# Optimization experiments

Hardware: AMD Instinct MI355X
Metric: run time of the kernel (lower is better)

## Reference

```python
import jax, jax.numpy as jnp
import numpy as np
from jax import lax

B, L, D = 2, 1024, 1024
INTER = 2816  # _find_multiple(round(4.0*1024*2/3), 256)
K, PAD = 3, 1
S = 32  # sqrt(L)
K2 = K * K


def setup_inputs() -> dict:
    key = jax.random.key(0)
    ks = jax.random.split(key, 7)
    x = jax.random.normal(ks[0], (B, L, D), dtype=jnp.float32)
    w_gate_up = jax.random.normal(ks[1], (2 * INTER, D), dtype=jnp.float32) / np.sqrt(D)
    w_metric = jax.random.normal(ks[2], (7, INTER, 3, 3), dtype=jnp.float32) / np.sqrt(INTER * 9)
    b_metric = jax.random.normal(ks[3], (7,), dtype=jnp.float32) * 0.01
    conv_w = jax.random.normal(ks[4], (INTER, 1, K, K), dtype=jnp.float32) / K
    conv_b = jnp.zeros((INTER,), dtype=jnp.float32)
    w_down = jax.random.normal(ks[5], (D, INTER), dtype=jnp.float32) / np.sqrt(INTER)
    return {"x": x, "w_gate_up": w_gate_up, "w_metric": w_metric,
            "b_metric": b_metric, "conv_w": conv_w, "conv_b": conv_b,
            "w_down": w_down}


def _metric_offsets(x2d, w_metric, b_metric):
    # Finsler-Randers style metric: 2x2 linear map M, drift vector, tanh scale.
    p = lax.conv_general_dilated(x2d, w_metric, (1, 1), 'SAME',
                                 dimension_numbers=('NCHW', 'OIHW', 'NCHW'))
    p = p + b_metric[None, :, None, None]  # [B,7,S,S]
    m00, m01, m10, m11 = p[:, 0], p[:, 1], p[:, 2], p[:, 3]
    dr_y, dr_x = p[:, 4], p[:, 5]
    scale = jnp.tanh(p[:, 6])
    ky = (jnp.arange(K) - PAD).astype(x2d.dtype)
    py = jnp.repeat(ky, K)   # (K2,) kernel-tap dy
    px = jnp.tile(ky, K)     # (K2,) kernel-tap dx
    pyb = py[None, :, None, None]
    pxb = px[None, :, None, None]
    off_y = scale[:, None] * (m00[:, None] * pyb + m01[:, None] * pxb) + dr_y[:, None]
    off_x = scale[:, None] * (m10[:, None] * pyb + m11[:, None] * pxb) + dr_x[:, None]
    return off_y, off_x, py, px  # offsets: [B,K2,S,S]


def _deform_depthwise(x2d, off_y, off_x, py, px, conv_w, conv_b):
    # Sampling positions per output pixel & kernel tap: [B,K2,S,S]
    iy = jnp.arange(S, dtype=x2d.dtype)
    pos_y = iy[None, None, :, None] + py[None, :, None, None] + off_y
    pos_x = iy[None, None, None, :] + px[None, :, None, None] + off_x
    y0 = jnp.floor(pos_y)
    x0 = jnp.floor(pos_x)
    ty = pos_y - y0
    tx = pos_x - x0
    y0i = y0.astype(jnp.int32)
    x0i = x0.astype(jnp.int32)
    flat = x2d.reshape(B, INTER, S * S)

    def corner(yy, xx):
        valid = ((yy >= 0) & (yy < S) & (xx >= 0) & (xx < S)).astype(x2d.dtype)
        idx = (jnp.clip(yy, 0, S - 1) * S + jnp.clip(xx, 0, S - 1)).reshape(B, 1, -1)
        v = jnp.take_along_axis(flat, idx, axis=2).reshape(B, INTER, K2, S, S)
        return v * valid[:, None]

    w00 = ((1 - ty) * (1 - tx))[:, None]
    w01 = ((1 - ty) * tx)[:, None]
    w10 = (ty * (1 - tx))[:, None]
    w11 = (ty * tx)[:, None]
    acc = w00 * corner(y0i, x0i)
    acc = acc + w01 * corner(y0i, x0i + 1)
    acc = acc + w10 * corner(y0i + 1, x0i)
    acc = acc + w11 * corner(y0i + 1, x0i + 1)
    out = jnp.einsum('bckij,ck->bcij', acc, conv_w.reshape(INTER, K2))
    return out + conv_b[None, :, None, None]


def reference(x, w_gate_up, w_metric, b_metric, conv_w, conv_b, w_down):
    gu = jnp.einsum('bld,fd->blf', x, w_gate_up)          # [B,L,2*inter]
    gate, up = jnp.split(gu, 2, axis=-1)
    x_ffn = jax.nn.silu(gate) * up                         # [B,L,inter]
    x2d = x_ffn.transpose(0, 2, 1).reshape(B, INTER, S, S)
    off_y, off_x, py, px = _metric_offsets(x2d, w_metric, b_metric)
    out2d = _deform_depthwise(x2d, off_y, off_x, py, px, conv_w, conv_b)
    grid_out = out2d.reshape(B, INTER, L).transpose(0, 2, 1)
    return jnp.einsum('blf,df->bld', grid_out, w_down)
```

## Files before the change

### kernel.cpp

```cpp
#include <hip/hip_runtime.h>
#include <hip/hip_bf16.h>
#include <cstdint>
#include <cstddef>
#include <type_traits>

#define INTER 2816

typedef __bf16 bf16x8 __attribute__((ext_vector_type(8)));
typedef float f32x4 __attribute__((ext_vector_type(4)));
typedef unsigned short u16x8 __attribute__((ext_vector_type(8)));
using bf16 = __hip_bfloat16;
using u16 = unsigned short;

__device__ __forceinline__ u16 f2bu(float f) {
  bf16 h = __float2bfloat16(f);
  return *reinterpret_cast<u16*>(&h);
}
__device__ __forceinline__ float bu2f(u16 u) {
  bf16 h = *reinterpret_cast<bf16*>(&u);
  return __bfloat162float(h);
}

__device__ __forceinline__ void async16(const u16* g, u16* l) {
  __builtin_amdgcn_global_load_lds(
      (const __attribute__((address_space(1))) unsigned int*)g,
      (__attribute__((address_space(3))) unsigned int*)l, 16, 0, 0);
}

__device__ __forceinline__ void stage8(u16* dst, const float* src) {
  const float4 a = *(const float4*)(src);
  const float4 b = *(const float4*)(src + 4);
  u16 tmp[8] = {f2bu(a.x), f2bu(a.y), f2bu(a.z), f2bu(a.w),
                f2bu(b.x), f2bu(b.y), f2bu(b.z), f2bu(b.w)};
  *(uint4*)dst = *(uint4*)tmp;
}

__global__ __launch_bounds__(256)
void prep_all(const float* __restrict__ x, const float* __restrict__ wgu,
              const float* __restrict__ wd, const float* __restrict__ w_metric,
              const float* __restrict__ conv_w, u16* __restrict__ xbf,
              u16* __restrict__ wgubf, u16* __restrict__ wdbf,
              u16* __restrict__ wm2, u16* __restrict__ cwb) {
  constexpr size_t S0 = (size_t)2048 * 1024;
  constexpr size_t S1 = (size_t)5632 * 1024;
  constexpr size_t S2 = (size_t)1024 * 2816;
  constexpr size_t NCONV_THREADS = (S0 + S1 + S2) / 8;
  const size_t t = (size_t)blockIdx.x * 256 + threadIdx.x;
  if (t < NCONV_THREADS) {
    const size_t e0 = t * 8;
    const float* src;
    u16* dst;
    size_t off;
    if (e0 < S0) {
      src = x; dst = xbf; off = e0;
    } else if (e0 < S0 + S1) {
      src = wgu; dst = wgubf; off = e0 - S0;
    } else {
      src = wd; dst = wdbf; off = e0 - S0 - S1;
    }
    stage8(dst + off, src + off);
  } else {
    const unsigned p = (unsigned)(t - NCONV_THREADS);
    const unsigned y = p / 2816u;
    const unsigned c = p - y * 2816u;
    if (y < 64) {
      float v = 0.f;
      if (y < 63) {
        const unsigned o = y / 9, tap = y - o * 9;
        v = w_metric[((size_t)o * INTER + c) * 9 + tap];
      }
      wm2[(size_t)y * INTER + c] = f2bu(v);
    } else {
      const unsigned k = y - 64;
      cwb[(size_t)k * INTER + c] = f2bu(conv_w[(size_t)c * 9 + k]);
    }
  }
}

template <int BN, bool NSWAP, typename OT>
__global__ __launch_bounds__(256, 3)
void gemm_nt(const u16* __restrict__ A, int lda, const u16* __restrict__ Bt,
             int ldb, OT* __restrict__ C, int M, int ldc, int K) {
  constexpr int NJ = BN / 32;
  __shared__ u16 As[2][128 * 32];
  __shared__ u16 Bs[2][BN * 32];
  const size_t koff = (size_t)blockIdx.z * K;
  A += koff;
  Bt += koff;
  C += (size_t)blockIdx.z * M * ldc;
  const int m0 = (NSWAP ? blockIdx.y : blockIdx.x) * 128;
  const int n0 = (NSWAP ? blockIdx.x : blockIdx.y) * BN;
  const int tid = threadIdx.x;
  const int lane = tid & 63;
  const int wv = tid >> 6;
  const int wm = wv & 1, wn = wv >> 1;
  const int lr = lane & 15;
  const int lq = lane >> 4;

  f32x4 acc[4][NJ];
#pragma unroll
  for (int i = 0; i < 4; ++i)
#pragma unroll
    for (int j = 0; j < NJ; ++j) acc[i][j] = (f32x4){0.f, 0.f, 0.f, 0.f};

  const int srow = tid >> 2;
  const int scol = (tid & 3) * 8;
  const u16* gA0 = A + (size_t)(m0 + srow) * lda + scol;
  const u16* gA1 = A + (size_t)(m0 + 64 + srow) * lda + scol;
  const u16* gB0 = Bt + (size_t)(n0 + srow) * ldb + scol;
  const u16* gB1 = Bt + (size_t)(n0 + 64 + srow) * ldb + scol;

  const int nIter = K >> 5;
  async16(gA0, &As[0][tid * 8]);
  async16(gA1, &As[0][2048 + tid * 8]);
  async16(gB0, &Bs[0][tid * 8]);
  if constexpr (BN == 128) async16(gB1, &Bs[0][2048 + tid * 8]);

  for (int it = 0; it < nIter; ++it) {
    __syncthreads();
    const int cur = it & 1;
    const u16* as = As[cur];
    const u16* bs = Bs[cur];
    if (it + 1 < nIter) {
      const int kb = (it + 1) << 5;
      const int nxt = cur ^ 1;
      async16(gA0 + kb, &As[nxt][tid * 8]);
      async16(gA1 + kb, &As[nxt][2048 + tid * 8]);
      async16(gB0 + kb, &Bs[nxt][tid * 8]);
      if constexpr (BN == 128) async16(gB1 + kb, &Bs[nxt][2048 + tid * 8]);
    }
    bf16x8 af[4], bfr[NJ];
#pragma unroll
    for (int i = 0; i < 4; ++i)
      af[i] = *(const bf16x8*)(&as[(wm * 64 + i * 16 + lr) * 32 + lq * 8]);
#pragma unroll
    for (int j = 0; j < NJ; ++j)
      bfr[j] = *(const bf16x8*)(&bs[(wn * (BN / 2) + j * 16 + lr) * 32 + lq * 8]);
#pragma unroll
    for (int i = 0; i < 4; ++i)
#pragma unroll
      for (int j = 0; j < NJ; ++j)
        acc[i][j] = __builtin_amdgcn_mfma_f32_16x16x32_bf16(af[i], bfr[j],
                                                            acc[i][j], 0, 0, 0);
  }

#pragma unroll
  for (int i = 0; i < 4; ++i)
#pragma unroll
    for (int j = 0; j < NJ; ++j) {
      const int col = n0 + wn * (BN / 2) + j * 16 + lr;
#pragma unroll
      for (int r = 0; r < 4; ++r) {
        const int row = m0 + wm * 64 + i * 16 + lq * 4 + r;
        const float v = acc[i][j][r];
        if constexpr (std::is_same_v<OT, float>) {
          C[(size_t)row * ldc + col] = v;
        } else {
          C[(size_t)row * ldc + col] = f2bu(v);
        }
      }
    }
}

__global__ void reduce4(const float* __restrict__ q2, float* __restrict__ out) {
  const size_t i = ((size_t)blockIdx.x * 256 + threadIdx.x) * 4;
  const size_t S = (size_t)2048 * 1024;
  float4 a = *(const float4*)(q2 + i);
  const float4 b = *(const float4*)(q2 + S + i);
  const float4 c = *(const float4*)(q2 + 2 * S + i);
  const float4 d = *(const float4*)(q2 + 3 * S + i);
  a.x += b.x + c.x + d.x;
  a.y += b.y + c.y + d.y;
  a.z += b.z + c.z + d.z;
  a.w += b.w + c.w + d.w;
  *(float4*)(out + i) = a;
}

__global__ __launch_bounds__(256, 2)
void gateup_gemm(const u16* __restrict__ x, const u16* __restrict__ wgu,
                 u16* __restrict__ xffn) {
  constexpr int K = 1024;
  __shared__ u16 As[2][128 * 32];
  __shared__ u16 Bgs[2][64 * 32];
  __shared__ u16 Bus[2][64 * 32];
  const int n0 = blockIdx.x * 64;
  const int m0 = blockIdx.y * 128;
  const int tid = threadIdx.x;
  const int lane = tid & 63;
  const int wv = tid >> 6;
  const int wm = wv & 1, wn = wv >> 1;
  const int lr = lane & 15;
  const int lq = lane >> 4;

  f32x4 accg[4][2], accu[4][2];
#pragma unroll
  for (int i = 0; i < 4; ++i)
#pragma unroll
    for (int j = 0; j < 2; ++j) {
      accg[i][j] = (f32x4){0.f, 0.f, 0.f, 0.f};
      accu[i][j] = (f32x4){0.f, 0.f, 0.f, 0.f};
    }

  const int srow = tid >> 2;
  const int scol = (tid & 3) * 8;
  const u16* gA0 = x + (size_t)(m0 + srow) * K + scol;
  const u16* gA1 = x + (size_t)(m0 + 64 + srow) * K + scol;
  const u16* gBg = wgu + (size_t)(n0 + srow) * K + scol;
  const u16* gBu = wgu + (size_t)(INTER + n0 + srow) * K + scol;

  constexpr int nIter = K >> 5;
  async16(gA0, &As[0][tid * 8]);
  async16(gA1, &As[0][2048 + tid * 8]);
  async16(gBg, &Bgs[0][tid * 8]);
  async16(gBu, &Bus[0][tid * 8]);

  for (int it = 0; it < nIter; ++it) {
    __syncthreads();
    const int cur = it & 1;
    const u16* as = As[cur];
    const u16* bgs = Bgs[cur];
    const u16* bus = Bus[cur];
    if (it + 1 < nIter) {
      const int kb = (it + 1) << 5;
      const int nxt = cur ^ 1;
      async16(gA0 + kb, &As[nxt][tid * 8]);
      async16(gA1 + kb, &As[nxt][2048 + tid * 8]);
      async16(gBg + kb, &Bgs[nxt][tid * 8]);
      async16(gBu + kb, &Bus[nxt][tid * 8]);
    }
    bf16x8 af[4], bg[2], bu[2];
#pragma unroll
    for (int i = 0; i < 4; ++i)
      af[i] = *(const bf16x8*)(&as[(wm * 64 + i * 16 + lr) * 32 + lq * 8]);
#pragma unroll
    for (int j = 0; j < 2; ++j) {
      bg[j] = *(const bf16x8*)(&bgs[(wn * 32 + j * 16 + lr) * 32 + lq * 8]);
      bu[j] = *(const bf16x8*)(&bus[(wn * 32 + j * 16 + lr) * 32 + lq * 8]);
    }
#pragma unroll
    for (int i = 0; i < 4; ++i)
#pragma unroll
      for (int j = 0; j < 2; ++j) {
        accg[i][j] = __builtin_amdgcn_mfma_f32_16x16x32_bf16(af[i], bg[j],
                                                             accg[i][j], 0, 0, 0);
        accu[i][j] = __builtin_amdgcn_mfma_f32_16x16x32_bf16(af[i], bu[j],
                                                             accu[i][j], 0, 0, 0);
      }
  }

#pragma unroll
  for (int i = 0; i < 4; ++i)
#pragma unroll
    for (int j = 0; j < 2; ++j) {
      const int col = n0 + wn * 32 + j * 16 + lr;
#pragma unroll
      for (int r = 0; r < 4; ++r) {
        const int row = m0 + wm * 64 + i * 16 + lq * 4 + r;
        const float g = accg[i][j][r];
        const float u = accu[i][j][r];
        const float s = g / (1.f + __expf(-g));
        xffn[(size_t)row * INTER + col] = f2bu(s * u);
      }
    }
}

__global__ __launch_bounds__(64)
void offsets_fused(const float* __restrict__ q,
                   const float* __restrict__ b_metric,
                   float4* __restrict__ wrec, int4* __restrict__ orec) {
  __shared__ float lds[130 * 65];
  const int chunk = blockIdx.x;
  const int b = chunk >> 4;
  const int c0 = (chunk & 15) * 64;
  const int t = threadIdx.x;

  for (int v = t; v < 130 * 16; v += 64) {
    const int row = v >> 4;
    const int c4 = (v & 15) * 4;
    int pg = c0 - 33 + row;
    pg = min(max(pg, 0), 1023);
    const float* src = q + ((size_t)b * 1024 + pg) * 64 + c4;
    float4 s = *(const float4*)(src);
#pragma unroll
    for (int ks = 1; ks < 8; ++ks) {
      const float4 vv = *(const float4*)(src + (size_t)ks * 2048 * 64);
      s.x += vv.x; s.y += vv.y; s.z += vv.z; s.w += vv.w;
    }
    float* d = &lds[row * 65 + c4];
    d[0] = s.x; d[1] = s.y; d[2] = s.z; d[3] = s.w;
  }
  __syncthreads();

  const int pix = c0 + t;
  const int i = pix >> 5, j = pix & 31;
  float p[7];
#pragma unroll
  for (int o = 0; o < 7; ++o) p[o] = b_metric[o];
#pragma unroll
  for (int tap = 0; tap < 9; ++tap) {
    const int dy = tap / 3 - 1, dx = tap % 3 - 1;
    const int ii = i + dy, jj = j + dx;
    if ((unsigned)ii < 32u && (unsigned)jj < 32u) {
      const float* r = &lds[(t + 33 + dy * 32 + dx) * 65 + tap];
#pragma unroll
      for (int o = 0; o < 7; ++o) p[o] += r[o * 9];
    }
  }
  const float m00 = p[0], m01 = p[1], m10 = p[2], m11 = p[3];
  const float dry = p[4], drx = p[5];
  const float sc = tanhf(p[6]);
#pragma unroll
  for (int k = 0; k < 9; ++k) {
    const float pyk = (float)(k / 3 - 1), pxk = (float)(k % 3 - 1);
    const float offy = sc * (m00 * pyk + m01 * pxk) + dry;
    const float offx = sc * (m10 * pyk + m11 * pxk) + drx;
    const float posy = (float)i + pyk + offy;
    const float posx = (float)j + pxk + offx;
    const float y0f = floorf(posy), x0f = floorf(posx);
    const int y0 = (int)y0f, x0 = (int)x0f;
    const float ty = posy - y0f, tx = posx - x0f;
    const int y1 = y0 + 1, x1 = x0 + 1;
    const float vy0 = ((unsigned)y0 < 32u) ? 1.f : 0.f;
    const float vy1 = ((unsigned)y1 < 32u) ? 1.f : 0.f;
    const float vx0 = ((unsigned)x0 < 32u) ? 1.f : 0.f;
    const float vx1 = ((unsigned)x1 < 32u) ? 1.f : 0.f;
    float4 w;
    w.x = (1.f - ty) * (1.f - tx) * vy0 * vx0;
    w.y = (1.f - ty) * tx * vy0 * vx1;
    w.z = ty * (1.f - tx) * vy1 * vx0;
    w.w = ty * tx * vy1 * vx1;
    const int cy0 = min(max(y0, 0), 31), cy1 = min(max(y1, 0), 31);
    const int cx0 = min(max(x0, 0), 31), cx1 = min(max(x1, 0), 31);
    int4 o;
    o.x = (cy0 * 32 + cx0) * (INTER * 2);
    o.y = (cy0 * 32 + cx1) * (INTER * 2);
    o.z = (cy1 * 32 + cx0) * (INTER * 2);
    o.w = (cy1 * 32 + cx1) * (INTER * 2);
    const size_t r = (((size_t)b * 9 + k) << 10) + pix;
    wrec[r] = w;
    orec[r] = o;
  }
}

__global__ __launch_bounds__(256)
void deform_kernel(const u16* __restrict__ xffn,
                   const float4* __restrict__ wrec,
                   const int4* __restrict__ orec,
                   const u16* __restrict__ cwb,
                   const float* __restrict__ conv_b,
                   u16* __restrict__ gridout) {
  const unsigned t = blockIdx.x * 256 + threadIdx.x;
  const unsigned pix = t / 352u;
  const unsigned cv = t - pix * 352u;
  const int c0 = cv * 8;
  const int b = pix >> 10, l = pix & 1023;

  float acc[8];
  {
    const float4 b0 = *(const float4*)(&conv_b[c0]);
    const float4 b1 = *(const float4*)(&conv_b[c0 + 4]);
    acc[0] = b0.x; acc[1] = b0.y; acc[2] = b0.z; acc[3] = b0.w;
    acc[4] = b1.x; acc[5] = b1.y; acc[6] = b1.z; acc[7] = b1.w;
  }
  const char* xb = (const char*)xffn +
                   ((size_t)b * 1024 * INTER + c0) * sizeof(u16);
#pragma unroll
  for (int k = 0; k < 9; ++k) {
    const size_t r = (((size_t)b * 9 + k) << 10) + l;
    const float4 w = wrec[r];
    const int4 o = orec[r];
    const u16x8 v00 = *(const u16x8*)(xb + o.x);
    const u16x8 v01 = *(const u16x8*)(xb + o.y);
    const u16x8 v10 = *(const u16x8*)(xb + o.z);
    const u16x8 v11 = *(const u16x8*)(xb + o.w);
    const u16x8 cw = *(const u16x8*)(&cwb[(size_t)k * INTER + c0]);
#pragma unroll
    for (int e = 0; e < 8; ++e) {
      const float bl = w.x * bu2f(v00[e]) + w.y * bu2f(v01[e]) +
                       w.z * bu2f(v10[e]) + w.w * bu2f(v11[e]);
      acc[e] += bl * bu2f(cw[e]);
    }
  }
  u16 outv[8];
#pragma unroll
  for (int e = 0; e < 8; ++e) outv[e] = f2bu(acc[e]);
  *(uint4*)(gridout + ((size_t)b * 1024 + l) * INTER + c0) = *(uint4*)outv;
}

extern "C" void kernel_launch(void* const* d_in, const int* in_sizes, int n_in,
                              void* d_out, int out_size, void* d_ws,
                              size_t ws_size, hipStream_t stream) {
  const float* x         = (const float*)d_in[0];
  const float* w_gate_up = (const float*)d_in[1];
  const float* w_metric  = (const float*)d_in[2];
  const float* b_metric  = (const float*)d_in[3];
  const float* conv_w    = (const float*)d_in[4];
  const float* conv_b    = (const float*)d_in[5];
  const float* w_down    = (const float*)d_in[6];
  float* out = (float*)d_out;

  char* w = (char*)d_ws;
  u16* gridout  = (u16*)(w);
  float* q2     = (float*)(w + (12u << 20));
  u16* xffn     = (u16*)(w + (12u << 20));
  u16* xbf      = (u16*)(w + (24u << 20));
  u16* wgubf    = (u16*)(w + (28u << 20) + (256u << 10));
  float* q_conv = (float*)(w + (28u << 20) + (256u << 10));
  u16* wm2      = (u16*)(w + (40u << 20));
  u16* cwb      = (u16*)(w + (41u << 20));
  float4* wrec  = (float4*)(w + (42u << 20));
  int4* orec    = (int4*)(w + (43u << 20));
  u16* wdbf     = (u16*)(w + (44u << 20));

  prep_all<<<6051, 256, 0, stream>>>(x, w_gate_up, w_down, w_metric, conv_w,
                                     xbf, wgubf, wdbf, wm2, cwb);
  gateup_gemm<<<dim3(44, 16), 256, 0, stream>>>(xbf, wgubf, xffn);
  gemm_nt<64, false, float><<<dim3(16, 1, 8), 256, 0, stream>>>(
      xffn, INTER, wm2, INTER, q_conv, 2048, 64, 352);
  offsets_fused<<<32, 64, 0, stream>>>(q_conv, b_metric, wrec, orec);
  deform_kernel<<<2816, 256, 0, stream>>>(xffn, wrec, orec, cwb, conv_b,
                                          gridout);
  gemm_nt<128, true, float><<<dim3(8, 16, 4), 256, 0, stream>>>(
      gridout, INTER, wdbf, INTER, q2, 2048, 1024, 704);
  reduce4<<<2048, 256, 0, stream>>>(q2, out);
}
```

Before: 204.9 us.

## Restructure GEMM k-loops to 64-wide stages, retune split-K, remap deform blocks

Both GEMM kernels replace the double-buffered 32-wide prefetch pipeline with a loop that loads a 64-wide k slab, synchronizes, computes both halves, then synchronizes again. This halves the barrier count per k element but drops the overlap of global loads with MFMA work. The metric-conv GEMM moves from 8 to 11 split-K slices of 256 and the reduction in offsets_fused sums 11 partials to match. The deform kernel permutes its block index so that consecutively launched blocks are spread across pixel ranges, changing scheduling and cache locality.

```diff
diff --git a/kernel.cpp b/kernel.cpp
--- a/kernel.cpp
+++ b/kernel.cpp
@@ -82,8 +82,9 @@
 void gemm_nt(const u16* __restrict__ A, int lda, const u16* __restrict__ Bt,
              int ldb, OT* __restrict__ C, int M, int ldc, int K) {
   constexpr int NJ = BN / 32;
-  __shared__ u16 As[2][128 * 32];
-  __shared__ u16 Bs[2][BN * 32];
+  constexpr int BHALF = BN * 32;
+  __shared__ u16 As[2 * 128 * 32];
+  __shared__ u16 Bs[2 * BHALF];
   const size_t koff = (size_t)blockIdx.z * K;
   A += koff;
   Bt += koff;
@@ -110,38 +111,33 @@
   const u16* gB0 = Bt + (size_t)(n0 + srow) * ldb + scol;
   const u16* gB1 = Bt + (size_t)(n0 + 64 + srow) * ldb + scol;
 
-  const int nIter = K >> 5;
-  async16(gA0, &As[0][tid * 8]);
-  async16(gA1, &As[0][2048 + tid * 8]);
-  async16(gB0, &Bs[0][tid * 8]);
-  if constexpr (BN == 128) async16(gB1, &Bs[0][2048 + tid * 8]);
-
-  for (int it = 0; it < nIter; ++it) {
+  for (int kb = 0; kb < K; kb += 64) {
+#pragma unroll
+    for (int h = 0; h < 2; ++h) {
+      const int kh = kb + h * 32;
+      async16(gA0 + kh, As + h * 4096 + tid * 8);
+      async16(gA1 + kh, As + h * 4096 + 2048 + tid * 8);
+      async16(gB0 + kh, Bs + h * BHALF + tid * 8);
+      if constexpr (BN == 128) async16(gB1 + kh, Bs + h * BHALF + 2048 + tid * 8);
+    }
     __syncthreads();
-    const int cur = it & 1;
-    const u16* as = As[cur];
-    const u16* bs = Bs[cur];
-    if (it + 1 < nIter) {
-      const int kb = (it + 1) << 5;
-      const int nxt = cur ^ 1;
-      async16(gA0 + kb, &As[nxt][tid * 8]);
-      async16(gA1 + kb, &As[nxt][2048 + tid * 8]);
-      async16(gB0 + kb, &Bs[nxt][tid * 8]);
-      if constexpr (BN == 128) async16(gB1 + kb, &Bs[nxt][2048 + tid * 8]);
-    }
-    bf16x8 af[4], bfr[NJ];
-#pragma unroll
-    for (int i = 0; i < 4; ++i)
-      af[i] = *(const bf16x8*)(&as[(wm * 64 + i * 16 + lr) * 32 + lq * 8]);
-#pragma unroll
-    for (int j = 0; j < NJ; ++j)
-      bfr[j] = *(const bf16x8*)(&bs[(wn * (BN / 2) + j * 16 + lr) * 32 + lq * 8]);
-#pragma unroll
-    for (int i = 0; i < 4; ++i)
+#pragma unroll
+    for (int h = 0; h < 2; ++h) {
+      bf16x8 af[4], bfr[NJ];
+#pragma unroll
+      for (int i = 0; i < 4; ++i)
+        af[i] = *(const bf16x8*)(&As[h * 4096 + (wm * 64 + i * 16 + lr) * 32 + lq * 8]);
 #pragma unroll
       for (int j = 0; j < NJ; ++j)
-        acc[i][j] = __builtin_amdgcn_mfma_f32_16x16x32_bf16(af[i], bfr[j],
-                                                            acc[i][j], 0, 0, 0);
+        bfr[j] = *(const bf16x8*)(&Bs[h * BHALF + (wn * (BN / 2) + j * 16 + lr) * 32 + lq * 8]);
+#pragma unroll
+      for (int i = 0; i < 4; ++i)
+#pragma unroll
+        for (int j = 0; j < NJ; ++j)
+          acc[i][j] = __builtin_amdgcn_mfma_f32_16x16x32_bf16(af[i], bfr[j],
+                                                              acc[i][j], 0, 0, 0);
+    }
+    __syncthreads();
   }
 
 #pragma unroll
@@ -180,9 +176,9 @@
 void gateup_gemm(const u16* __restrict__ x, const u16* __restrict__ wgu,
                  u16* __restrict__ xffn) {
   constexpr int K = 1024;
-  __shared__ u16 As[2][128 * 32];
-  __shared__ u16 Bgs[2][64 * 32];
-  __shared__ u16 Bus[2][64 * 32];
+  __shared__ u16 As[2 * 128 * 32];
+  __shared__ u16 Bgs[2 * 64 * 32];
+  __shared__ u16 Bus[2 * 64 * 32];
   const int n0 = blockIdx.x * 64;
   const int m0 = blockIdx.y * 128;
   const int tid = threadIdx.x;
@@ -208,44 +204,38 @@
   const u16* gBg = wgu + (size_t)(n0 + srow) * K + scol;
   const u16* gBu = wgu + (size_t)(INTER + n0 + srow) * K + scol;
 
-  constexpr int nIter = K >> 5;
-  async16(gA0, &As[0][tid * 8]);
-  async16(gA1, &As[0][2048 + tid * 8]);
-  async16(gBg, &Bgs[0][tid * 8]);
-  async16(gBu, &Bus[0][tid * 8]);
-
-  for (int it = 0; it < nIter; ++it) {
+  for (int kb = 0; kb < K; kb += 64) {
+#pragma unroll
+    for (int h = 0; h < 2; ++h) {
+      const int kh = kb + h * 32;
+      async16(gA0 + kh, As + h * 4096 + tid * 8);
+      async16(gA1 + kh, As + h * 4096 + 2048 + tid * 8);
+      async16(gBg + kh, Bgs + h * 2048 + tid * 8);
+      async16(gBu + kh, Bus + h * 2048 + tid * 8);
+    }
     __syncthreads();
-    const int cur = it & 1;
-    const u16* as = As[cur];
-    const u16* bgs = Bgs[cur];
-    const u16* bus = Bus[cur];
-    if (it + 1 < nIter) {
-      const int kb = (it + 1) << 5;
-      const int nxt = cur ^ 1;
-      async16(gA0 + kb, &As[nxt][tid * 8]);
-      async16(gA1 + kb, &As[nxt][2048 + tid * 8]);
-      async16(gBg + kb, &Bgs[nxt][tid * 8]);
-      async16(gBu + kb, &Bus[nxt][tid * 8]);
-    }
-    bf16x8 af[4], bg[2], bu[2];
-#pragma unroll
-    for (int i = 0; i < 4; ++i)
-      af[i] = *(const bf16x8*)(&as[(wm * 64 + i * 16 + lr) * 32 + lq * 8]);
-#pragma unroll
-    for (int j = 0; j < 2; ++j) {
-      bg[j] = *(const bf16x8*)(&bgs[(wn * 32 + j * 16 + lr) * 32 + lq * 8]);
-      bu[j] = *(const bf16x8*)(&bus[(wn * 32 + j * 16 + lr) * 32 + lq * 8]);
-    }
-#pragma unroll
-    for (int i = 0; i < 4; ++i)
+#pragma unroll
+    for (int h = 0; h < 2; ++h) {
+      bf16x8 af[4], bg[2], bu[2];
+#pragma unroll
+      for (int i = 0; i < 4; ++i)
+        af[i] = *(const bf16x8*)(&As[h * 4096 + (wm * 64 + i * 16 + lr) * 32 + lq * 8]);
 #pragma unroll
       for (int j = 0; j < 2; ++j) {
-        accg[i][j] = __builtin_amdgcn_mfma_f32_16x16x32_bf16(af[i], bg[j],
-                                                             accg[i][j], 0, 0, 0);
-        accu[i][j] = __builtin_amdgcn_mfma_f32_16x16x32_bf16(af[i], bu[j],
-                                                             accu[i][j], 0, 0, 0);
+        bg[j] = *(const bf16x8*)(&Bgs[h * 2048 + (wn * 32 + j * 16 + lr) * 32 + lq * 8]);
+        bu[j] = *(const bf16x8*)(&Bus[h * 2048 + (wn * 32 + j * 16 + lr) * 32 + lq * 8]);
       }
+#pragma unroll
+      for (int i = 0; i < 4; ++i)
+#pragma unroll
+        for (int j = 0; j < 2; ++j) {
+          accg[i][j] = __builtin_amdgcn_mfma_f32_16x16x32_bf16(af[i], bg[j],
+                                                               accg[i][j], 0, 0, 0);
+          accu[i][j] = __builtin_amdgcn_mfma_f32_16x16x32_bf16(af[i], bu[j],
+                                                               accu[i][j], 0, 0, 0);
+        }
+    }
+    __syncthreads();
   }
 
 #pragma unroll
@@ -282,7 +272,7 @@
     const float* src = q + ((size_t)b * 1024 + pg) * 64 + c4;
     float4 s = *(const float4*)(src);
 #pragma unroll
-    for (int ks = 1; ks < 8; ++ks) {
+    for (int ks = 1; ks < 11; ++ks) {
       const float4 vv = *(const float4*)(src + (size_t)ks * 2048 * 64);
       s.x += vv.x; s.y += vv.y; s.z += vv.z; s.w += vv.w;
     }
@@ -349,7 +339,8 @@
                    const u16* __restrict__ cwb,
                    const float* __restrict__ conv_b,
                    u16* __restrict__ gridout) {
-  const unsigned t = blockIdx.x * 256 + threadIdx.x;
+  const unsigned bid = (blockIdx.x & 7u) * 352u + (blockIdx.x >> 3);
+  const unsigned t = bid * 256 + threadIdx.x;
   const unsigned pix = t / 352u;
   const unsigned cv = t - pix * 352u;
   const int c0 = cv * 8;
@@ -415,8 +406,8 @@
   prep_all<<<6051, 256, 0, stream>>>(x, w_gate_up, w_down, w_metric, conv_w,
                                      xbf, wgubf, wdbf, wm2, cwb);
   gateup_gemm<<<dim3(44, 16), 256, 0, stream>>>(xbf, wgubf, xffn);
-  gemm_nt<64, false, float><<<dim3(16, 1, 8), 256, 0, stream>>>(
-      xffn, INTER, wm2, INTER, q_conv, 2048, 64, 352);
+  gemm_nt<64, false, float><<<dim3(16, 1, 11), 256, 0, stream>>>(
+      xffn, INTER, wm2, INTER, q_conv, 2048, 64, 256);
   offsets_fused<<<32, 64, 0, stream>>>(q_conv, b_metric, wrec, orec);
   deform_kernel<<<2816, 256, 0, stream>>>(xffn, wrec, orec, cwb, conv_b,
                                           gridout);
```

Result: no change. 203.1 us (-0.9%).
